# Performance work log

Hardware: AMD Instinct MI355X
Metric: run time of the kernel (lower is better)

Reference implementation:

```python
import jax, jax.numpy as jnp
import numpy as np

N_NODES = 100000


def _gcn_conv(x, W, b, src, dst, norm, num_nodes):
    # PyG GCNConv: h = x @ W; out = scatter_add(norm_e * h[src] -> dst) + b
    h = x @ W                               # [N, out]
    msgs = h[src] * norm[:, None]           # [E', out]
    agg = jax.ops.segment_sum(msgs, dst, num_segments=num_nodes)
    return agg + b


def _gcn_norm(edge_index, num_nodes):
    # add self-loops, then sym-normalize: deg^-1/2[src] * deg^-1/2[dst]
    loops = jnp.arange(num_nodes, dtype=edge_index.dtype)
    src = jnp.concatenate([edge_index[0], loops])
    dst = jnp.concatenate([edge_index[1], loops])
    deg = jax.ops.segment_sum(jnp.ones_like(dst, dtype=jnp.float32), dst,
                              num_segments=num_nodes)
    dis = jnp.where(deg > 0, jax.lax.rsqrt(jnp.maximum(deg, 1.0)), 0.0)
    norm = dis[src] * dis[dst]              # [E + N]
    return src, dst, norm


def setup_inputs() -> dict:
    key = jax.random.key(0)
    k1, k2, k3, k4 = jax.random.split(key, 4)
    in_feat, hidden, n_classes = 512, 16, 16
    n_edges = 3200000
    x = jax.random.normal(k1, (N_NODES, in_feat), dtype=jnp.float32)
    edge_index = jax.random.randint(k2, (2, n_edges), 0, N_NODES, dtype=jnp.int64)
    W1 = jax.random.normal(k3, (in_feat, hidden), dtype=jnp.float32) / np.sqrt(in_feat)
    b1 = jnp.zeros((hidden,), dtype=jnp.float32)
    W2 = jax.random.normal(k4, (hidden, n_classes), dtype=jnp.float32) / np.sqrt(hidden)
    b2 = jnp.zeros((n_classes,), dtype=jnp.float32)
    return {"x": x, "edge_index": edge_index, "W1": W1, "b1": b1, "W2": W2, "b2": b2}


def reference(x, edge_index, W1, b1, W2, b2):
    num_nodes = x.shape[0]
    src, dst, norm = _gcn_norm(edge_index, num_nodes)
    h = _gcn_conv(x, W1, b1, src, dst, norm, num_nodes)
    h = jax.nn.relu(h)
    # dropout is identity at inference (training=False)
    h = _gcn_conv(h, W2, b2, src, dst, norm, num_nodes)
    return jax.nn.log_softmax(h, axis=1)
```

## Files before the change

### kernel.cpp

```cpp
#include <hip/hip_runtime.h>
#include <hip/hip_bf16.h>
#include <math.h>

#define NNODES 100000
#define NBUCK 8
#define XRANGE 12500
#define NCHUNK 32
#define CAP 408192
#define BCHUNK 6250

typedef __attribute__((ext_vector_type(8))) short bf16x8;
typedef __attribute__((ext_vector_type(4))) float f32x4;

__device__ __forceinline__ float bflo(unsigned int u) {
  union { unsigned int i; float f; } v; v.i = u << 16; return v.f;
}
__device__ __forceinline__ float bfhi(unsigned int u) {
  union { unsigned int i; float f; } v; v.i = u & 0xFFFF0000u; return v.f;
}
__device__ __forceinline__ unsigned int f2bf1(float f) {
  union { float f; unsigned int i; } v; v.f = f;
  return (v.i + 0x7FFFu + ((v.i >> 16) & 1u)) >> 16;
}
__device__ __forceinline__ unsigned int f2bf2(float a, float b) {
  return f2bf1(a) | (f2bf1(b) << 16);
}

__device__ __forceinline__ int edge_val(const void* eidx, int is64, size_t i) {
  if (is64) return (int)((const long long*)eidx)[i];
  return ((const int*)eidx)[i];
}

__global__ void k_init(const void* eidx, int* flag, int* gcur) {
  int t = threadIdx.x;
  int bad = 0;
  const unsigned long long* p = (const unsigned long long*)eidx;
  for (int i = t; i < 1024; i += 64)
    if (p[i] >> 32) bad = 1;
  unsigned long long b = __ballot(bad);
  if (t == 0) flag[0] = (b == 0ULL) ? 1 : 0;
  if (t < NBUCK) gcur[t] = 0;
}

__global__ void k_bin(const void* eidx, const int* __restrict__ flag, int* gcur,
                      int* __restrict__ sArr, unsigned short* __restrict__ dArr, int E) {
  __shared__ unsigned int s_sb[BCHUNK];
  __shared__ unsigned short s_dl[BCHUNK];
  __shared__ int bbase[NBUCK], lcur[NBUCK], wcnt[4][NBUCK];
  int is64 = flag[0];
  int beg = blockIdx.x * BCHUNK;
  int end = min(beg + BCHUNK, E);
  int cnt = end - beg;
  int lane = threadIdx.x & 63, wid = threadIdx.x >> 6;

  int cl = 0;
  for (int i = threadIdx.x; i < cnt; i += 256) {
    int e = beg + i;
    int s = edge_val(eidx, is64, e);
    int d = edge_val(eidx, is64, (size_t)E + e);
    int bk = d / XRANGE;
    s_sb[i] = (unsigned int)s | ((unsigned int)bk << 17);
    s_dl[i] = (unsigned short)(d - bk * XRANGE);
    #pragma unroll
    for (int b = 0; b < NBUCK; ++b) {
      unsigned long long m = __ballot(bk == b);
      if (lane == b) cl += __popcll(m);
    }
  }
  if (lane < NBUCK) wcnt[wid][lane] = cl;
  __syncthreads();
  if (threadIdx.x < NBUCK) {
    int t = wcnt[0][threadIdx.x] + wcnt[1][threadIdx.x] +
            wcnt[2][threadIdx.x] + wcnt[3][threadIdx.x];
    bbase[threadIdx.x] = atomicAdd(&gcur[threadIdx.x], t);
    lcur[threadIdx.x] = 0;
  }
  __syncthreads();

  for (int i = threadIdx.x; i < cnt; i += 256) {
    unsigned int sb = s_sb[i];
    int bk = (int)(sb >> 17);
    int s = (int)(sb & 0x1FFFFu);
    unsigned short dl = s_dl[i];
    #pragma unroll
    for (int b = 0; b < NBUCK; ++b) {
      unsigned long long m = __ballot(bk == b);
      int c = __popcll(m);
      if (!c) continue;
      int leader = __ffsll((unsigned long long)m) - 1;
      int base = 0;
      if (lane == leader) base = atomicAdd(&lcur[b], c);
      base = __shfl(base, leader);
      if (bk == b) {
        int rank = __popcll(m & ((1ULL << lane) - 1));
        int gpos = bbase[b] + base + rank;
        if (gpos < CAP) {
          sArr[(size_t)b * CAP + gpos] = s;
          dArr[(size_t)b * CAP + gpos] = dl;
        }
      }
    }
  }
}

__global__ void k_hist(const int* __restrict__ gcur, const unsigned short* __restrict__ dArr,
                       int* __restrict__ cntc) {
  int b = blockIdx.x & (NBUCK - 1);
  int c = blockIdx.x >> 3;
  __shared__ int h[XRANGE];
  for (int i = threadIdx.x; i < XRANGE; i += 256) h[i] = 0;
  __syncthreads();
  int nE = min(gcur[b], CAP);
  int ce = (nE + NCHUNK - 1) / NCHUNK;
  int beg = c * ce, end = min(beg + ce, nE);
  const unsigned short* dp = dArr + (size_t)b * CAP;
  for (int e = beg + threadIdx.x; e < end; e += 256)
    atomicAdd(&h[dp[e]], 1);
  __syncthreads();
  int lo = b * XRANGE;
  for (int i = threadIdx.x; i < XRANGE; i += 256)
    cntc[(size_t)c * NNODES + lo + i] = h[i];
}

__global__ void k_dis(const int* __restrict__ cntc, int* __restrict__ tot,
                      float* __restrict__ dis, int* __restrict__ bsum, int n) {
  int i = blockIdx.x * 256 + threadIdx.x;
  int t = 0;
  if (i < n) {
    #pragma unroll
    for (int c = 0; c < NCHUNK; ++c) t += cntc[(size_t)c * NNODES + i];
    tot[i] = t;
    dis[i] = rsqrtf((float)(t + 1));
  }
  int v = t;
  #pragma unroll
  for (int d = 32; d > 0; d >>= 1) v += __shfl_down(v, d);
  __shared__ int ws4[4];
  if ((threadIdx.x & 63) == 0) ws4[threadIdx.x >> 6] = v;
  __syncthreads();
  if (threadIdx.x == 0) bsum[blockIdx.x] = ws4[0] + ws4[1] + ws4[2] + ws4[3];
}

__global__ void k_scan_fc(const int* __restrict__ tot, const int* __restrict__ bsum,
                          int* __restrict__ rowptr, int* __restrict__ cntc, int n, int nb) {
  __shared__ int ps[512];
  __shared__ int s[256];
  int t = threadIdx.x;
  ps[t] = (t < nb) ? bsum[t] : 0;
  ps[t + 256] = (t + 256 < nb) ? bsum[t + 256] : 0;
  __syncthreads();
  for (int d = 1; d < 512; d <<= 1) {
    int u0 = (t >= d) ? ps[t - d] : 0;
    int u1 = (t + 256 >= d) ? ps[t + 256 - d] : 0;
    __syncthreads();
    ps[t] += u0;
    ps[t + 256] += u1;
    __syncthreads();
  }
  int bex = (blockIdx.x == 0) ? 0 : ps[blockIdx.x - 1];
  if (blockIdx.x == 0 && t == 0) rowptr[n] = ps[nb - 1];

  int idx = blockIdx.x * 256 + t;
  int v = (idx < n) ? tot[idx] : 0;
  s[t] = v;
  __syncthreads();
  for (int d = 1; d < 256; d <<= 1) {
    int u = (t >= d) ? s[t - d] : 0;
    __syncthreads();
    s[t] += u;
    __syncthreads();
  }
  if (idx < n) {
    int run = bex + s[t] - v;
    rowptr[idx] = run;
    #pragma unroll
    for (int c = 0; c < NCHUNK; ++c) {
      size_t id2 = (size_t)c * NNODES + idx;
      int tc = cntc[id2];
      cntc[id2] = run;
      run += tc;
    }
  }
}

__global__ void k_scatter(const int* __restrict__ gcur, const int* __restrict__ sArr,
                          const unsigned short* __restrict__ dArr,
                          const int* __restrict__ cntc, int* __restrict__ col) {
  int b = blockIdx.x & (NBUCK - 1);
  int c = blockIdx.x >> 3;
  __shared__ int cur[XRANGE];
  int lo = b * XRANGE;
  for (int i = threadIdx.x; i < XRANGE; i += 256)
    cur[i] = cntc[(size_t)c * NNODES + lo + i];
  __syncthreads();
  int nE = min(gcur[b], CAP);
  int ce = (nE + NCHUNK - 1) / NCHUNK;
  int beg = c * ce, end = min(beg + ce, nE);
  const int* sp = sArr + (size_t)b * CAP;
  const unsigned short* dp = dArr + (size_t)b * CAP;
  for (int e = beg + threadIdx.x; e < end; e += 256) {
    int d = dp[e];
    int pos = atomicAdd(&cur[d], 1);
    col[pos] = sp[e];
  }
}

__device__ __forceinline__ bf16x8 cvt8(const float4& p, const float4& q) {
  union { unsigned int u[4]; bf16x8 v; } r;
  r.u[0] = f2bf2(p.x, p.y);
  r.u[1] = f2bf2(p.z, p.w);
  r.u[2] = f2bf2(q.x, q.y);
  r.u[3] = f2bf2(q.z, q.w);
  return r.v;
}

__device__ __forceinline__ bf16x8 cvtW(const float* wf) {
  union { unsigned int u[4]; bf16x8 v; } r;
  r.u[0] = f2bf2(wf[0], wf[1]);
  r.u[1] = f2bf2(wf[2], wf[3]);
  r.u[2] = f2bf2(wf[4], wf[5]);
  r.u[3] = f2bf2(wf[6], wf[7]);
  return r.v;
}

__global__ __launch_bounds__(64, 4) void k_gemm1(const float* __restrict__ x,
                                                 const float* __restrict__ W,
                                                 const float* __restrict__ dis,
                                                 unsigned short* __restrict__ gb, int nrows) {
  int lane = threadIdx.x;
  int row0 = blockIdx.x * 32;
  int q8 = lane >> 4;
  int jm = lane & 15;
  const float4* x4 = (const float4*)x;
  size_t xb0 = (size_t)(row0 + jm) * 128 + q8 * 2;
  size_t xb1 = (size_t)(row0 + 16 + jm) * 128 + q8 * 2;

  float4 va0 = x4[xb0], va1 = x4[xb0 + 1];
  float4 va2 = x4[xb1], va3 = x4[xb1 + 1];
  float wf[8];
  #pragma unroll
  for (int i = 0; i < 8; ++i)
    wf[i] = W[(size_t)(q8 * 8 + i) * 16 + jm];

  f32x4 acc0 = {0.f, 0.f, 0.f, 0.f}, acc1 = {0.f, 0.f, 0.f, 0.f};

  #pragma unroll
  for (int kc = 0; kc < 16; ++kc) {
    float4 vn0, vn1, vn2, vn3;
    float wn[8];
    if (kc + 1 < 16) {
      vn0 = x4[xb0 + (kc + 1) * 8];
      vn1 = x4[xb0 + (kc + 1) * 8 + 1];
      vn2 = x4[xb1 + (kc + 1) * 8];
      vn3 = x4[xb1 + (kc + 1) * 8 + 1];
      #pragma unroll
      for (int i = 0; i < 8; ++i)
        wn[i] = W[(size_t)((kc + 1) * 32 + q8 * 8 + i) * 16 + jm];
    }
    bf16x8 bfr = cvtW(wf);
    acc0 = __builtin_amdgcn_mfma_f32_16x16x32_bf16(cvt8(va0, va1), bfr, acc0, 0, 0, 0);
    acc1 = __builtin_amdgcn_mfma_f32_16x16x32_bf16(cvt8(va2, va3), bfr, acc1, 0, 0, 0);
    if (kc + 1 < 16) {
      va0 = vn0; va1 = vn1; va2 = vn2; va3 = vn3;
      #pragma unroll
      for (int i = 0; i < 8; ++i) wf[i] = wn[i];
    }
  }

  float dis_own = dis[row0 + min(lane, 31)];
  #pragma unroll
  for (int r = 0; r < 4; ++r) {
    int rl0 = q8 * 4 + r;
    float d0 = __shfl(dis_own, rl0);
    gb[(size_t)(row0 + rl0) * 16 + jm] = (unsigned short)f2bf1(acc0[r] * d0);
    int rl1 = 16 + rl0;
    float d1 = __shfl(dis_own, rl1);
    gb[(size_t)(row0 + rl1) * 16 + jm] = (unsigned short)f2bf1(acc1[r] * d1);
  }
}

__global__ void k_gemm2(const float* __restrict__ o1, const float* __restrict__ W,
                        const float* __restrict__ dis, unsigned int* __restrict__ gb, int nrows) {
  int row = blockIdx.x * blockDim.x + threadIdx.x;
  if (row >= nrows) return;
  const float4* xr = (const float4*)(o1 + (size_t)row * 16);
  float4 x0 = xr[0], x1 = xr[1], x2 = xr[2], x3 = xr[3];
  float xv[16] = {x0.x, x0.y, x0.z, x0.w, x1.x, x1.y, x1.z, x1.w,
                  x2.x, x2.y, x2.z, x2.w, x3.x, x3.y, x3.z, x3.w};
  float acc[16];
  #pragma unroll
  for (int j = 0; j < 16; ++j) acc[j] = 0.f;
  #pragma unroll
  for (int k = 0; k < 16; ++k) {
    const float* wr = W + (size_t)k * 16;
    #pragma unroll
    for (int j = 0; j < 16; ++j)
      acc[j] = fmaf(xv[k], wr[j], acc[j]);
  }
  float dd = dis[row];
  uint4 pa, pb;
  pa.x = f2bf2(acc[0] * dd, acc[1] * dd);
  pa.y = f2bf2(acc[2] * dd, acc[3] * dd);
  pa.z = f2bf2(acc[4] * dd, acc[5] * dd);
  pa.w = f2bf2(acc[6] * dd, acc[7] * dd);
  pb.x = f2bf2(acc[8] * dd, acc[9] * dd);
  pb.y = f2bf2(acc[10] * dd, acc[11] * dd);
  pb.z = f2bf2(acc[12] * dd, acc[13] * dd);
  pb.w = f2bf2(acc[14] * dd, acc[15] * dd);
  uint4* g4 = (uint4*)gb;
  g4[(size_t)row * 2] = pa;
  g4[(size_t)row * 2 + 1] = pb;
}

__device__ __forceinline__ void gather8v2(const uint4* gp, const int* __restrict__ col,
                                          int beg, int end, int h, int slot, float* acc) {
  #pragma unroll
  for (int j = 0; j < 8; ++j) acc[j] = 0.f;
  for (int e = beg + slot; e < end; e += 16) {
    int s = col[e];
    uint4 v = gp[(size_t)s * 2 + h];
    acc[0] += bflo(v.x); acc[1] += bfhi(v.x);
    acc[2] += bflo(v.y); acc[3] += bfhi(v.y);
    acc[4] += bflo(v.z); acc[5] += bfhi(v.z);
    acc[6] += bflo(v.w); acc[7] += bfhi(v.w);
  }
  #pragma unroll
  for (int d = 2; d < 32; d <<= 1) {
    #pragma unroll
    for (int j = 0; j < 8; ++j) acc[j] += __shfl_xor(acc[j], d);
  }
}

__global__ void k_agg1(const unsigned int* __restrict__ gb, const int* __restrict__ col,
                       const int* __restrict__ rowptr, const float* __restrict__ dis,
                       const float* __restrict__ bias, float* __restrict__ o1) {
  int wid = threadIdx.x >> 6;
  int lane = threadIdx.x & 63;
  int n2 = lane >> 5;
  int node = blockIdx.x * 8 + wid * 2 + n2;
  if (node >= NNODES) return;
  int rem = lane & 31;
  int h = rem & 1, slot = rem >> 1;
  const uint4* gp = (const uint4*)gb;
  float acc[8];
  gather8v2(gp, col, rowptr[node], rowptr[node + 1], h, slot, acc);
  uint4 sv = gp[(size_t)node * 2 + h];
  acc[0] += bflo(sv.x); acc[1] += bfhi(sv.x);
  acc[2] += bflo(sv.y); acc[3] += bfhi(sv.y);
  acc[4] += bflo(sv.z); acc[5] += bfhi(sv.z);
  acc[6] += bflo(sv.w); acc[7] += bfhi(sv.w);
  float dd = dis[node];
  const float4* b4 = (const float4*)bias;
  float4 ba = b4[2 * h], bb = b4[2 * h + 1];
  float z0 = fmaxf(fmaf(dd, acc[0], ba.x), 0.f);
  float z1 = fmaxf(fmaf(dd, acc[1], ba.y), 0.f);
  float z2 = fmaxf(fmaf(dd, acc[2], ba.z), 0.f);
  float z3 = fmaxf(fmaf(dd, acc[3], ba.w), 0.f);
  float z4 = fmaxf(fmaf(dd, acc[4], bb.x), 0.f);
  float z5 = fmaxf(fmaf(dd, acc[5], bb.y), 0.f);
  float z6 = fmaxf(fmaf(dd, acc[6], bb.z), 0.f);
  float z7 = fmaxf(fmaf(dd, acc[7], bb.w), 0.f);
  if (slot == 0) {
    float4* o4 = (float4*)o1;
    o4[(size_t)node * 4 + 2 * h] = make_float4(z0, z1, z2, z3);
    o4[(size_t)node * 4 + 2 * h + 1] = make_float4(z4, z5, z6, z7);
  }
}

__global__ void k_agg2(const unsigned int* __restrict__ gb, const int* __restrict__ col,
                       const int* __restrict__ rowptr, const float* __restrict__ dis,
                       const float* __restrict__ bias, float* __restrict__ out) {
  int wid = threadIdx.x >> 6;
  int lane = threadIdx.x & 63;
  int n2 = lane >> 5;
  int node = blockIdx.x * 8 + wid * 2 + n2;
  if (node >= NNODES) return;
  int rem = lane & 31;
  int h = rem & 1, slot = rem >> 1;
  const uint4* gp = (const uint4*)gb;
  float acc[8];
  gather8v2(gp, col, rowptr[node], rowptr[node + 1], h, slot, acc);
  uint4 sv = gp[(size_t)node * 2 + h];
  acc[0] += bflo(sv.x); acc[1] += bfhi(sv.x);
  acc[2] += bflo(sv.y); acc[3] += bfhi(sv.y);
  acc[4] += bflo(sv.z); acc[5] += bfhi(sv.z);
  acc[6] += bflo(sv.w); acc[7] += bfhi(sv.w);
  float dd = dis[node];
  const float4* b4 = (const float4*)bias;
  float4 ba = b4[2 * h], bb = b4[2 * h + 1];
  float z[8];
  z[0] = fmaf(dd, acc[0], ba.x); z[1] = fmaf(dd, acc[1], ba.y);
  z[2] = fmaf(dd, acc[2], ba.z); z[3] = fmaf(dd, acc[3], ba.w);
  z[4] = fmaf(dd, acc[4], bb.x); z[5] = fmaf(dd, acc[5], bb.y);
  z[6] = fmaf(dd, acc[6], bb.z); z[7] = fmaf(dd, acc[7], bb.w);
  float m = z[0];
  #pragma unroll
  for (int j = 1; j < 8; ++j) m = fmaxf(m, z[j]);
  m = fmaxf(m, __shfl_xor(m, 1));
  float se = 0.f;
  #pragma unroll
  for (int j = 0; j < 8; ++j) se += expf(z[j] - m);
  se += __shfl_xor(se, 1);
  float lg = m + logf(se);
  if (slot == 0) {
    float4* o4 = (float4*)out;
    o4[(size_t)node * 4 + 2 * h] = make_float4(z[0] - lg, z[1] - lg, z[2] - lg, z[3] - lg);
    o4[(size_t)node * 4 + 2 * h + 1] = make_float4(z[4] - lg, z[5] - lg, z[6] - lg, z[7] - lg);
  }
}

extern "C" void kernel_launch(void* const* d_in, const int* in_sizes, int n_in,
                              void* d_out, int out_size, void* d_ws, size_t ws_size,
                              hipStream_t stream) {
  const float* x  = (const float*)d_in[0];
  const void*  ei = d_in[1];
  const float* W1 = (const float*)d_in[2];
  const float* b1 = (const float*)d_in[3];
  const float* W2 = (const float*)d_in[4];
  const float* b2 = (const float*)d_in[5];
  float* out = (float*)d_out;

  const int n = NNODES;
  const int E = in_sizes[1] / 2;

  char* ws = (char*)d_ws;
  size_t off = 0;
  auto alloc = [&](size_t bytes) -> void* {
    void* p = ws + off;
    off = (off + bytes + 255) & ~(size_t)255;
    return p;
  };
  int*            flag   = (int*)            alloc(256);
  int*            gcur   = (int*)            alloc(256);
  int*            sArr   = (int*)            alloc((size_t)NBUCK * CAP * 4);
  unsigned short* dArr   = (unsigned short*) alloc((size_t)NBUCK * CAP * 2);
  int*            cntc   = (int*)            alloc((size_t)NCHUNK * n * 4);
  int*            tot    = (int*)            alloc((size_t)n * 4);
  float*          dis    = (float*)          alloc((size_t)n * 4);
  int*            rowptr = (int*)            alloc((size_t)(n + 1) * 4);
  int*            bsum   = (int*)            alloc(4096);
  int*            col    = (int*)            alloc((size_t)E * 4);
  unsigned short* gb1    = (unsigned short*) alloc((size_t)n * 16 * 2);
  float*          o1  = (float*)sArr;
  unsigned int*   gb2 = (unsigned int*)dArr;
  (void)ws_size; (void)n_in; (void)out_size;

  int nb = (n + 255) / 256;

  k_init<<<1, 64, 0, stream>>>(ei, flag, gcur);
  k_bin<<<(E + BCHUNK - 1) / BCHUNK, 256, 0, stream>>>(ei, flag, gcur, sArr, dArr, E);
  k_hist<<<NBUCK * NCHUNK, 256, 0, stream>>>(gcur, dArr, cntc);
  k_dis<<<nb, 256, 0, stream>>>(cntc, tot, dis, bsum, n);

  k_gemm1<<<n / 32, 64, 0, stream>>>(x, W1, dis, gb1, n);

  k_scan_fc<<<nb, 256, 0, stream>>>(tot, bsum, rowptr, cntc, n, nb);
  k_scatter<<<NBUCK * NCHUNK, 256, 0, stream>>>(gcur, sArr, dArr, cntc, col);

  k_agg1<<<(n + 7) / 8, 256, 0, stream>>>((const unsigned int*)gb1, col, rowptr, dis, b1, o1);
  k_gemm2<<<(n + 255) / 256, 256, 0, stream>>>(o1, W2, dis, gb2, n);
  k_agg2<<<(n + 7) / 8, 256, 0, stream>>>(gb2, col, rowptr, dis, b2, out);
}
```

Before: 237.1 us.

## Fuse layer-2 GEMM into first aggregation; shrink GEMM1 tiles and bin chunks

The second small 16x16 GEMM is folded into the epilogue of the first aggregation kernel. Each half-row lane multiplies its 8 ReLU outputs by its half of W2, the two partial results are combined with a lane shuffle, and the result is written as scaled bf16 straight to gb2. This removes one kernel launch and the fp32 o1 round trip through memory. GEMM1 now handles 16 rows per block instead of 32 and drops the manual software prefetch, which doubles the grid and raises the launch-bounds occupancy hint. The binning chunk size is halved, giving more blocks.

```diff
diff --git a/kernel.cpp b/kernel.cpp
--- a/kernel.cpp
+++ b/kernel.cpp
@@ -7,7 +7,7 @@
 #define XRANGE 12500
 #define NCHUNK 32
 #define CAP 408192
-#define BCHUNK 6250
+#define BCHUNK 3125
 
 typedef __attribute__((ext_vector_type(8))) short bf16x8;
 typedef __attribute__((ext_vector_type(4))) float f32x4;
@@ -223,93 +223,36 @@
   return r.v;
 }
 
-__global__ __launch_bounds__(64, 4) void k_gemm1(const float* __restrict__ x,
+__global__ __launch_bounds__(64, 8) void k_gemm1(const float* __restrict__ x,
                                                  const float* __restrict__ W,
                                                  const float* __restrict__ dis,
                                                  unsigned short* __restrict__ gb, int nrows) {
   int lane = threadIdx.x;
-  int row0 = blockIdx.x * 32;
+  int row0 = blockIdx.x * 16;
   int q8 = lane >> 4;
   int jm = lane & 15;
   const float4* x4 = (const float4*)x;
-  size_t xb0 = (size_t)(row0 + jm) * 128 + q8 * 2;
-  size_t xb1 = (size_t)(row0 + 16 + jm) * 128 + q8 * 2;
-
-  float4 va0 = x4[xb0], va1 = x4[xb0 + 1];
-  float4 va2 = x4[xb1], va3 = x4[xb1 + 1];
-  float wf[8];
-  #pragma unroll
-  for (int i = 0; i < 8; ++i)
-    wf[i] = W[(size_t)(q8 * 8 + i) * 16 + jm];
-
-  f32x4 acc0 = {0.f, 0.f, 0.f, 0.f}, acc1 = {0.f, 0.f, 0.f, 0.f};
-
+  size_t xb = (size_t)(row0 + jm) * 128 + q8 * 2;
+
+  f32x4 acc = {0.f, 0.f, 0.f, 0.f};
   #pragma unroll
   for (int kc = 0; kc < 16; ++kc) {
-    float4 vn0, vn1, vn2, vn3;
-    float wn[8];
-    if (kc + 1 < 16) {
-      vn0 = x4[xb0 + (kc + 1) * 8];
-      vn1 = x4[xb0 + (kc + 1) * 8 + 1];
-      vn2 = x4[xb1 + (kc + 1) * 8];
-      vn3 = x4[xb1 + (kc + 1) * 8 + 1];
-      #pragma unroll
-      for (int i = 0; i < 8; ++i)
-        wn[i] = W[(size_t)((kc + 1) * 32 + q8 * 8 + i) * 16 + jm];
-    }
-    bf16x8 bfr = cvtW(wf);
-    acc0 = __builtin_amdgcn_mfma_f32_16x16x32_bf16(cvt8(va0, va1), bfr, acc0, 0, 0, 0);
-    acc1 = __builtin_amdgcn_mfma_f32_16x16x32_bf16(cvt8(va2, va3), bfr, acc1, 0, 0, 0);
-    if (kc + 1 < 16) {
-      va0 = vn0; va1 = vn1; va2 = vn2; va3 = vn3;
-      #pragma unroll
-      for (int i = 0; i < 8; ++i) wf[i] = wn[i];
-    }
-  }
-
-  float dis_own = dis[row0 + min(lane, 31)];
+    float4 v0 = x4[xb + kc * 8];
+    float4 v1 = x4[xb + kc * 8 + 1];
+    float wf[8];
+    #pragma unroll
+    for (int i = 0; i < 8; ++i)
+      wf[i] = W[(size_t)(kc * 32 + q8 * 8 + i) * 16 + jm];
+    acc = __builtin_amdgcn_mfma_f32_16x16x32_bf16(cvt8(v0, v1), cvtW(wf), acc, 0, 0, 0);
+  }
+
+  float dis_own = dis[row0 + min(lane, 15)];
   #pragma unroll
   for (int r = 0; r < 4; ++r) {
-    int rl0 = q8 * 4 + r;
-    float d0 = __shfl(dis_own, rl0);
-    gb[(size_t)(row0 + rl0) * 16 + jm] = (unsigned short)f2bf1(acc0[r] * d0);
-    int rl1 = 16 + rl0;
-    float d1 = __shfl(dis_own, rl1);
-    gb[(size_t)(row0 + rl1) * 16 + jm] = (unsigned short)f2bf1(acc1[r] * d1);
-  }
-}
-
-__global__ void k_gemm2(const float* __restrict__ o1, const float* __restrict__ W,
-                        const float* __restrict__ dis, unsigned int* __restrict__ gb, int nrows) {
-  int row = blockIdx.x * blockDim.x + threadIdx.x;
-  if (row >= nrows) return;
-  const float4* xr = (const float4*)(o1 + (size_t)row * 16);
-  float4 x0 = xr[0], x1 = xr[1], x2 = xr[2], x3 = xr[3];
-  float xv[16] = {x0.x, x0.y, x0.z, x0.w, x1.x, x1.y, x1.z, x1.w,
-                  x2.x, x2.y, x2.z, x2.w, x3.x, x3.y, x3.z, x3.w};
-  float acc[16];
-  #pragma unroll
-  for (int j = 0; j < 16; ++j) acc[j] = 0.f;
-  #pragma unroll
-  for (int k = 0; k < 16; ++k) {
-    const float* wr = W + (size_t)k * 16;
-    #pragma unroll
-    for (int j = 0; j < 16; ++j)
-      acc[j] = fmaf(xv[k], wr[j], acc[j]);
-  }
-  float dd = dis[row];
-  uint4 pa, pb;
-  pa.x = f2bf2(acc[0] * dd, acc[1] * dd);
-  pa.y = f2bf2(acc[2] * dd, acc[3] * dd);
-  pa.z = f2bf2(acc[4] * dd, acc[5] * dd);
-  pa.w = f2bf2(acc[6] * dd, acc[7] * dd);
-  pb.x = f2bf2(acc[8] * dd, acc[9] * dd);
-  pb.y = f2bf2(acc[10] * dd, acc[11] * dd);
-  pb.z = f2bf2(acc[12] * dd, acc[13] * dd);
-  pb.w = f2bf2(acc[14] * dd, acc[15] * dd);
-  uint4* g4 = (uint4*)gb;
-  g4[(size_t)row * 2] = pa;
-  g4[(size_t)row * 2 + 1] = pb;
+    int rloc = q8 * 4 + r;
+    float dd = __shfl(dis_own, rloc);
+    gb[(size_t)(row0 + rloc) * 16 + jm] = (unsigned short)f2bf1(acc[r] * dd);
+  }
 }
 
 __device__ __forceinline__ void gather8v2(const uint4* gp, const int* __restrict__ col,
@@ -333,7 +276,8 @@
 
 __global__ void k_agg1(const unsigned int* __restrict__ gb, const int* __restrict__ col,
                        const int* __restrict__ rowptr, const float* __restrict__ dis,
-                       const float* __restrict__ bias, float* __restrict__ o1) {
+                       const float* __restrict__ bias, const float* __restrict__ W2,
+                       unsigned int* __restrict__ gb2) {
   int wid = threadIdx.x >> 6;
   int lane = threadIdx.x & 63;
   int n2 = lane >> 5;
@@ -352,18 +296,36 @@
   float dd = dis[node];
   const float4* b4 = (const float4*)bias;
   float4 ba = b4[2 * h], bb = b4[2 * h + 1];
-  float z0 = fmaxf(fmaf(dd, acc[0], ba.x), 0.f);
-  float z1 = fmaxf(fmaf(dd, acc[1], ba.y), 0.f);
-  float z2 = fmaxf(fmaf(dd, acc[2], ba.z), 0.f);
-  float z3 = fmaxf(fmaf(dd, acc[3], ba.w), 0.f);
-  float z4 = fmaxf(fmaf(dd, acc[4], bb.x), 0.f);
-  float z5 = fmaxf(fmaf(dd, acc[5], bb.y), 0.f);
-  float z6 = fmaxf(fmaf(dd, acc[6], bb.z), 0.f);
-  float z7 = fmaxf(fmaf(dd, acc[7], bb.w), 0.f);
+  float z[8];
+  z[0] = fmaxf(fmaf(dd, acc[0], ba.x), 0.f);
+  z[1] = fmaxf(fmaf(dd, acc[1], ba.y), 0.f);
+  z[2] = fmaxf(fmaf(dd, acc[2], ba.z), 0.f);
+  z[3] = fmaxf(fmaf(dd, acc[3], ba.w), 0.f);
+  z[4] = fmaxf(fmaf(dd, acc[4], bb.x), 0.f);
+  z[5] = fmaxf(fmaf(dd, acc[5], bb.y), 0.f);
+  z[6] = fmaxf(fmaf(dd, acc[6], bb.z), 0.f);
+  z[7] = fmaxf(fmaf(dd, acc[7], bb.w), 0.f);
   if (slot == 0) {
-    float4* o4 = (float4*)o1;
-    o4[(size_t)node * 4 + 2 * h] = make_float4(z0, z1, z2, z3);
-    o4[(size_t)node * 4 + 2 * h + 1] = make_float4(z4, z5, z6, z7);
+    float p[16];
+    #pragma unroll
+    for (int j = 0; j < 16; ++j) p[j] = 0.f;
+    #pragma unroll
+    for (int kk = 0; kk < 8; ++kk) {
+      const float* wr = W2 + (size_t)(h * 8 + kk) * 16;
+      float zk = z[kk];
+      #pragma unroll
+      for (int j = 0; j < 16; ++j)
+        p[j] = fmaf(zk, wr[j], p[j]);
+    }
+    #pragma unroll
+    for (int j = 0; j < 16; ++j) p[j] += __shfl_xor(p[j], 1);
+    uint4 pk;
+    int o = h * 8;
+    pk.x = f2bf2(p[o + 0] * dd, p[o + 1] * dd);
+    pk.y = f2bf2(p[o + 2] * dd, p[o + 3] * dd);
+    pk.z = f2bf2(p[o + 4] * dd, p[o + 5] * dd);
+    pk.w = f2bf2(p[o + 6] * dd, p[o + 7] * dd);
+    ((uint4*)gb2)[(size_t)node * 2 + h] = pk;
   }
 }
 
@@ -441,7 +403,6 @@
   int*            bsum   = (int*)            alloc(4096);
   int*            col    = (int*)            alloc((size_t)E * 4);
   unsigned short* gb1    = (unsigned short*) alloc((size_t)n * 16 * 2);
-  float*          o1  = (float*)sArr;
   unsigned int*   gb2 = (unsigned int*)dArr;
   (void)ws_size; (void)n_in; (void)out_size;
 
@@ -452,12 +413,11 @@
   k_hist<<<NBUCK * NCHUNK, 256, 0, stream>>>(gcur, dArr, cntc);
   k_dis<<<nb, 256, 0, stream>>>(cntc, tot, dis, bsum, n);
 
-  k_gemm1<<<n / 32, 64, 0, stream>>>(x, W1, dis, gb1, n);
+  k_gemm1<<<n / 16, 64, 0, stream>>>(x, W1, dis, gb1, n);
 
   k_scan_fc<<<nb, 256, 0, stream>>>(tot, bsum, rowptr, cntc, n, nb);
   k_scatter<<<NBUCK * NCHUNK, 256, 0, stream>>>(gcur, sArr, dArr, cntc, col);
 
-  k_agg1<<<(n + 7) / 8, 256, 0, stream>>>((const unsigned int*)gb1, col, rowptr, dis, b1, o1);
-  k_gemm2<<<(n + 255) / 256, 256, 0, stream>>>(o1, W2, dis, gb2, n);
+  k_agg1<<<(n + 7) / 8, 256, 0, stream>>>((const unsigned int*)gb1, col, rowptr, dis, b1, W2, gb2);
   k_agg2<<<(n + 7) / 8, 256, 0, stream>>>(gb2, col, rowptr, dis, b2, out);
 }
```

Measured after the change: 256.9 us. +8.3%, slower.

## Fuse GEMM1 into edge-binning kernel via block roles and defer dis scaling

Applied to the files above, without the earlier changes.

The x@W1 MFMA GEMM is merged into the edge-binning kernel, with blocks split 3:2 between GEMM tiles (four waves per block) and binning work. The aim is to overlap the compute-heavy GEMM with the memory-bound binning of edge_index, since the GEMM no longer waits for the degree computation. The per-row dis scaling moves into k_dis, which rescales the bf16 GEMM output in place. This adds an extra read-modify-write of gb1 and a second bf16 rounding step. The fused kernel's shared-memory footprint also applies to the GEMM blocks, which may reduce occupancy.

```diff
diff --git a/kernel.cpp b/kernel.cpp
--- a/kernel.cpp
+++ b/kernel.cpp
@@ -8,6 +8,7 @@
 #define NCHUNK 32
 #define CAP 408192
 #define BCHUNK 6250
+#define GTILES (NNODES / 32)
 
 typedef __attribute__((ext_vector_type(8))) short bf16x8;
 typedef __attribute__((ext_vector_type(4))) float f32x4;
@@ -29,6 +30,24 @@
 __device__ __forceinline__ int edge_val(const void* eidx, int is64, size_t i) {
   if (is64) return (int)((const long long*)eidx)[i];
   return ((const int*)eidx)[i];
+}
+
+__device__ __forceinline__ bf16x8 cvt8(const float4& p, const float4& q) {
+  union { unsigned int u[4]; bf16x8 v; } r;
+  r.u[0] = f2bf2(p.x, p.y);
+  r.u[1] = f2bf2(p.z, p.w);
+  r.u[2] = f2bf2(q.x, q.y);
+  r.u[3] = f2bf2(q.z, q.w);
+  return r.v;
+}
+
+__device__ __forceinline__ bf16x8 cvtW(const float* wf) {
+  union { unsigned int u[4]; bf16x8 v; } r;
+  r.u[0] = f2bf2(wf[0], wf[1]);
+  r.u[1] = f2bf2(wf[2], wf[3]);
+  r.u[2] = f2bf2(wf[4], wf[5]);
+  r.u[3] = f2bf2(wf[6], wf[7]);
+  return r.v;
 }
 
 __global__ void k_init(const void* eidx, int* flag, int* gcur) {
@@ -42,13 +61,73 @@
   if (t < NBUCK) gcur[t] = 0;
 }
 
-__global__ void k_bin(const void* eidx, const int* __restrict__ flag, int* gcur,
-                      int* __restrict__ sArr, unsigned short* __restrict__ dArr, int E) {
+__global__ void k_binmm(const void* eidx, const int* __restrict__ flag, int* gcur,
+                        int* __restrict__ sArr, unsigned short* __restrict__ dArr,
+                        int E, int binBlocks,
+                        const float* __restrict__ x, const float* __restrict__ W,
+                        unsigned short* __restrict__ gb, int gemmBlocks) {
   __shared__ unsigned int s_sb[BCHUNK];
   __shared__ unsigned short s_dl[BCHUNK];
   __shared__ int bbase[NBUCK], lcur[NBUCK], wcnt[4][NBUCK];
+
+  int grp = blockIdx.x / 5, role = blockIdx.x % 5;
+  if (role < 3) {
+    int gid = grp * 3 + role;
+    if (gid >= gemmBlocks) return;
+    int wid = threadIdx.x >> 6;
+    int tile = gid * 4 + wid;
+    if (tile >= GTILES) return;
+    int lane = threadIdx.x & 63;
+    int row0 = tile * 32;
+    int q8 = lane >> 4;
+    int jm = lane & 15;
+    const float4* x4 = (const float4*)x;
+    size_t xb0 = (size_t)(row0 + jm) * 128 + q8 * 2;
+    size_t xb1 = (size_t)(row0 + 16 + jm) * 128 + q8 * 2;
+
+    float4 va0 = x4[xb0], va1 = x4[xb0 + 1];
+    float4 va2 = x4[xb1], va3 = x4[xb1 + 1];
+    float wf[8];
+    #pragma unroll
+    for (int i = 0; i < 8; ++i)
+      wf[i] = W[(size_t)(q8 * 8 + i) * 16 + jm];
+
+    f32x4 acc0 = {0.f, 0.f, 0.f, 0.f}, acc1 = {0.f, 0.f, 0.f, 0.f};
+    #pragma unroll
+    for (int kc = 0; kc < 16; ++kc) {
+      float4 vn0, vn1, vn2, vn3;
+      float wn[8];
+      if (kc + 1 < 16) {
+        vn0 = x4[xb0 + (kc + 1) * 8];
+        vn1 = x4[xb0 + (kc + 1) * 8 + 1];
+        vn2 = x4[xb1 + (kc + 1) * 8];
+        vn3 = x4[xb1 + (kc + 1) * 8 + 1];
+        #pragma unroll
+        for (int i = 0; i < 8; ++i)
+          wn[i] = W[(size_t)((kc + 1) * 32 + q8 * 8 + i) * 16 + jm];
+      }
+      bf16x8 bfr = cvtW(wf);
+      acc0 = __builtin_amdgcn_mfma_f32_16x16x32_bf16(cvt8(va0, va1), bfr, acc0, 0, 0, 0);
+      acc1 = __builtin_amdgcn_mfma_f32_16x16x32_bf16(cvt8(va2, va3), bfr, acc1, 0, 0, 0);
+      if (kc + 1 < 16) {
+        va0 = vn0; va1 = vn1; va2 = vn2; va3 = vn3;
+        #pragma unroll
+        for (int i = 0; i < 8; ++i) wf[i] = wn[i];
+      }
+    }
+    #pragma unroll
+    for (int r = 0; r < 4; ++r) {
+      int rl0 = q8 * 4 + r;
+      gb[(size_t)(row0 + rl0) * 16 + jm] = (unsigned short)f2bf1(acc0[r]);
+      gb[(size_t)(row0 + 16 + rl0) * 16 + jm] = (unsigned short)f2bf1(acc1[r]);
+    }
+    return;
+  }
+
+  int bid = grp * 2 + (role - 3);
+  if (bid >= binBlocks) return;
   int is64 = flag[0];
-  int beg = blockIdx.x * BCHUNK;
+  int beg = bid * BCHUNK;
   int end = min(beg + BCHUNK, E);
   int cnt = end - beg;
   int lane = threadIdx.x & 63, wid = threadIdx.x >> 6;
@@ -123,14 +202,28 @@
 }
 
 __global__ void k_dis(const int* __restrict__ cntc, int* __restrict__ tot,
-                      float* __restrict__ dis, int* __restrict__ bsum, int n) {
+                      float* __restrict__ dis, int* __restrict__ bsum,
+                      unsigned int* __restrict__ gb1, int n) {
   int i = blockIdx.x * 256 + threadIdx.x;
   int t = 0;
   if (i < n) {
     #pragma unroll
     for (int c = 0; c < NCHUNK; ++c) t += cntc[(size_t)c * NNODES + i];
     tot[i] = t;
-    dis[i] = rsqrtf((float)(t + 1));
+    float dd = rsqrtf((float)(t + 1));
+    dis[i] = dd;
+    uint4* g4 = (uint4*)gb1;
+    uint4 pa = g4[(size_t)i * 2], pb = g4[(size_t)i * 2 + 1];
+    pa.x = f2bf2(bflo(pa.x) * dd, bfhi(pa.x) * dd);
+    pa.y = f2bf2(bflo(pa.y) * dd, bfhi(pa.y) * dd);
+    pa.z = f2bf2(bflo(pa.z) * dd, bfhi(pa.z) * dd);
+    pa.w = f2bf2(bflo(pa.w) * dd, bfhi(pa.w) * dd);
+    pb.x = f2bf2(bflo(pb.x) * dd, bfhi(pb.x) * dd);
+    pb.y = f2bf2(bflo(pb.y) * dd, bfhi(pb.y) * dd);
+    pb.z = f2bf2(bflo(pb.z) * dd, bfhi(pb.z) * dd);
+    pb.w = f2bf2(bflo(pb.w) * dd, bfhi(pb.w) * dd);
+    g4[(size_t)i * 2] = pa;
+    g4[(size_t)i * 2 + 1] = pb;
   }
   int v = t;
   #pragma unroll
@@ -202,80 +295,6 @@
     int d = dp[e];
     int pos = atomicAdd(&cur[d], 1);
     col[pos] = sp[e];
-  }
-}
-
-__device__ __forceinline__ bf16x8 cvt8(const float4& p, const float4& q) {
-  union { unsigned int u[4]; bf16x8 v; } r;
-  r.u[0] = f2bf2(p.x, p.y);
-  r.u[1] = f2bf2(p.z, p.w);
-  r.u[2] = f2bf2(q.x, q.y);
-  r.u[3] = f2bf2(q.z, q.w);
-  return r.v;
-}
-
-__device__ __forceinline__ bf16x8 cvtW(const float* wf) {
-  union { unsigned int u[4]; bf16x8 v; } r;
-  r.u[0] = f2bf2(wf[0], wf[1]);
-  r.u[1] = f2bf2(wf[2], wf[3]);
-  r.u[2] = f2bf2(wf[4], wf[5]);
-  r.u[3] = f2bf2(wf[6], wf[7]);
-  return r.v;
-}
-
-__global__ __launch_bounds__(64, 4) void k_gemm1(const float* __restrict__ x,
-                                                 const float* __restrict__ W,
-                                                 const float* __restrict__ dis,
-                                                 unsigned short* __restrict__ gb, int nrows) {
-  int lane = threadIdx.x;
-  int row0 = blockIdx.x * 32;
-  int q8 = lane >> 4;
-  int jm = lane & 15;
-  const float4* x4 = (const float4*)x;
-  size_t xb0 = (size_t)(row0 + jm) * 128 + q8 * 2;
-  size_t xb1 = (size_t)(row0 + 16 + jm) * 128 + q8 * 2;
-
-  float4 va0 = x4[xb0], va1 = x4[xb0 + 1];
-  float4 va2 = x4[xb1], va3 = x4[xb1 + 1];
-  float wf[8];
-  #pragma unroll
-  for (int i = 0; i < 8; ++i)
-    wf[i] = W[(size_t)(q8 * 8 + i) * 16 + jm];
-
-  f32x4 acc0 = {0.f, 0.f, 0.f, 0.f}, acc1 = {0.f, 0.f, 0.f, 0.f};
-
-  #pragma unroll
-  for (int kc = 0; kc < 16; ++kc) {
-    float4 vn0, vn1, vn2, vn3;
-    float wn[8];
-    if (kc + 1 < 16) {
-      vn0 = x4[xb0 + (kc + 1) * 8];
-      vn1 = x4[xb0 + (kc + 1) * 8 + 1];
-      vn2 = x4[xb1 + (kc + 1) * 8];
-      vn3 = x4[xb1 + (kc + 1) * 8 + 1];
-      #pragma unroll
-      for (int i = 0; i < 8; ++i)
-        wn[i] = W[(size_t)((kc + 1) * 32 + q8 * 8 + i) * 16 + jm];
-    }
-    bf16x8 bfr = cvtW(wf);
-    acc0 = __builtin_amdgcn_mfma_f32_16x16x32_bf16(cvt8(va0, va1), bfr, acc0, 0, 0, 0);
-    acc1 = __builtin_amdgcn_mfma_f32_16x16x32_bf16(cvt8(va2, va3), bfr, acc1, 0, 0, 0);
-    if (kc + 1 < 16) {
-      va0 = vn0; va1 = vn1; va2 = vn2; va3 = vn3;
-      #pragma unroll
-      for (int i = 0; i < 8; ++i) wf[i] = wn[i];
-    }
-  }
-
-  float dis_own = dis[row0 + min(lane, 31)];
-  #pragma unroll
-  for (int r = 0; r < 4; ++r) {
-    int rl0 = q8 * 4 + r;
-    float d0 = __shfl(dis_own, rl0);
-    gb[(size_t)(row0 + rl0) * 16 + jm] = (unsigned short)f2bf1(acc0[r] * d0);
-    int rl1 = 16 + rl0;
-    float d1 = __shfl(dis_own, rl1);
-    gb[(size_t)(row0 + rl1) * 16 + jm] = (unsigned short)f2bf1(acc1[r] * d1);
   }
 }
 
@@ -446,18 +465,20 @@
   (void)ws_size; (void)n_in; (void)out_size;
 
   int nb = (n + 255) / 256;
+  int binBlocks  = (E + BCHUNK - 1) / BCHUNK;
+  int gemmBlocks = (GTILES + 3) / 4;
+  int groups = max((gemmBlocks + 2) / 3, (binBlocks + 1) / 2);
+  int grid = groups * 5;
 
   k_init<<<1, 64, 0, stream>>>(ei, flag, gcur);
-  k_bin<<<(E + BCHUNK - 1) / BCHUNK, 256, 0, stream>>>(ei, flag, gcur, sArr, dArr, E);
+  k_binmm<<<grid, 256, 0, stream>>>(ei, flag, gcur, sArr, dArr, E, binBlocks,
+                                    x, W1, gb1, gemmBlocks);
   k_hist<<<NBUCK * NCHUNK, 256, 0, stream>>>(gcur, dArr, cntc);
-  k_dis<<<nb, 256, 0, stream>>>(cntc, tot, dis, bsum, n);
-
-  k_gemm1<<<n / 32, 64, 0, stream>>>(x, W1, dis, gb1, n);
-
+  k_dis<<<nb, 256, 0, stream>>>(cntc, tot, dis, bsum, (unsigned int*)gb1, n);
   k_scan_fc<<<nb, 256, 0, stream>>>(tot, bsum, rowptr, cntc, n, nb);
   k_scatter<<<NBUCK * NCHUNK, 256, 0, stream>>>(gcur, sArr, dArr, cntc, col);
 
   k_agg1<<<(n + 7) / 8, 256, 0, stream>>>((const unsigned int*)gb1, col, rowptr, dis, b1, o1);
-  k_gemm2<<<(n + 255) / 256, 256, 0, stream>>>(o1, W2, dis, gb2, n);
+  k_gemm2<<<(n + 255) / 256, 256, 0, stream>>>(o1, W2, dis, (unsigned int*)gb2, n);
   k_agg2<<<(n + 7) / 8, 256, 0, stream>>>(gb2, col, rowptr, dis, b2, out);
 }
```

After: 224.2 us. 1.06x faster.
